# Optimization experiments

Hardware: AMD Instinct MI355X
Metric: run time of the kernel (lower is better)

Reference implementation:

```python
import jax, jax.numpy as jnp
import numpy as np

B, S, D = 4, 1024, 1024
E, F, TOPK = 16, 512, 4


def setup_inputs() -> dict:
    key = jax.random.key(0)
    k1, k2, k3, k4, k5 = jax.random.split(key, 5)
    scale = 0.02
    return {
        "x": jax.random.normal(k1, (B, S, D), dtype=jnp.float32),
        "Wr": jax.random.normal(k2, (D, E), dtype=jnp.float32) * scale,   # router
        "Wg": jax.random.normal(k3, (E, D, F), dtype=jnp.float32) * scale,  # gate proj
        "Wu": jax.random.normal(k4, (E, D, F), dtype=jnp.float32) * scale,  # up proj
        "Wd": jax.random.normal(k5, (E, F, D), dtype=jnp.float32) * scale,  # down proj
    }


def reference(x, Wr, Wg, Wu, Wd):
    b, s, d = x.shape
    xf = x.reshape(-1, d)                      # [N, D], N = B*S
    n = xf.shape[0]
    e = Wr.shape[1]

    # --- router: softmax over experts, top-k, renormalized weights ---
    probs = jax.nn.softmax(xf @ Wr, axis=-1)   # [N, E]
    w, idx = jax.lax.top_k(probs, TOPK)        # [N, K], [N, K]
    w = w / jnp.sum(w, axis=-1, keepdims=True)

    # combine weights per (token, expert); zero for unselected experts.
    # Equivalent to the per-expert where/gather/scatter-add loop in torch.
    cw = jnp.zeros((n, e), dtype=xf.dtype).at[jnp.arange(n)[:, None], idx].add(w)

    # --- per-expert gated FFN (SwiGLU), combined with routing weights ---
    def body(acc, ws):
        wg, wu, wd, c = ws                     # [D,F], [D,F], [F,D], [N]
        h = jax.nn.silu(xf @ wg) * (xf @ wu)   # [N, F]
        return acc + c[:, None] * (h @ wd), None

    out, _ = jax.lax.scan(body, jnp.zeros_like(xf), (Wg, Wu, Wd, cw.T))
    return out.reshape(b, s, d)
```

## Files before the change

### kernel.cpp

```cpp
#include <hip/hip_runtime.h>

#define N_TOK 4096
#define DIM   1024
#define NE    16
#define NF    512
#define TOPK  4
#define CAP   4096
#define NPAIR (N_TOK * TOPK)
#define MAXTILES 144

typedef _Float16 v8h __attribute__((ext_vector_type(8)));
typedef float    v4f __attribute__((ext_vector_type(4)));

__global__ __launch_bounds__(64) void router_kernel(
    const float* __restrict__ x, const float* __restrict__ Wr,
    int* __restrict__ tokIdx, float* __restrict__ tokW,
    unsigned short* __restrict__ xb)
{
    int t = blockIdx.x;
    int l = threadIdx.x;
    double z[NE];
#pragma unroll
    for (int e = 0; e < NE; e++) z[e] = 0.0;
    const float* xrow = x + (size_t)t * DIM;
#pragma unroll
    for (int i = 0; i < 16; i++) {
        int d = i * 64 + l;
        double xv = (double)xrow[d];
        const float4* wr = (const float4*)(Wr + d * NE);
        float4 w0 = wr[0], w1 = wr[1], w2 = wr[2], w3 = wr[3];
        z[0]  += xv * w0.x; z[1]  += xv * w0.y; z[2]  += xv * w0.z; z[3]  += xv * w0.w;
        z[4]  += xv * w1.x; z[5]  += xv * w1.y; z[6]  += xv * w1.z; z[7]  += xv * w1.w;
        z[8]  += xv * w2.x; z[9]  += xv * w2.y; z[10] += xv * w2.z; z[11] += xv * w2.w;
        z[12] += xv * w3.x; z[13] += xv * w3.y; z[14] += xv * w3.z; z[15] += xv * w3.w;
    }
    const float4* xv4 = (const float4*)xrow;
#pragma unroll
    for (int h2 = 0; h2 < 2; h2++) {
        int base = h2 * 512 + l * 8;
        float4 a = xv4[h2 * 128 + l * 2];
        float4 b = xv4[h2 * 128 + l * 2 + 1];
        union { unsigned short u[8]; uint4 v; } p;
        p.u[0] = __builtin_bit_cast(unsigned short, (_Float16)a.x);
        p.u[1] = __builtin_bit_cast(unsigned short, (_Float16)a.y);
        p.u[2] = __builtin_bit_cast(unsigned short, (_Float16)a.z);
        p.u[3] = __builtin_bit_cast(unsigned short, (_Float16)a.w);
        p.u[4] = __builtin_bit_cast(unsigned short, (_Float16)b.x);
        p.u[5] = __builtin_bit_cast(unsigned short, (_Float16)b.y);
        p.u[6] = __builtin_bit_cast(unsigned short, (_Float16)b.z);
        p.u[7] = __builtin_bit_cast(unsigned short, (_Float16)b.w);
        *(uint4*)(xb + (size_t)t * DIM + base) = p.v;
    }
#pragma unroll
    for (int e = 0; e < NE; e++) {
#pragma unroll
        for (int m = 1; m < 64; m <<= 1) z[e] += __shfl_xor(z[e], m, 64);
    }
    if (l == 0) {
        bool taken[NE];
#pragma unroll
        for (int e = 0; e < NE; e++) taken[e] = false;
        int idx[TOPK]; double sel[TOPK];
        for (int k = 0; k < TOPK; k++) {
            int bi = 0; double bv = -1.0e300;
            for (int e = 0; e < NE; e++)
                if (!taken[e] && z[e] > bv) { bv = z[e]; bi = e; }
            taken[bi] = true; idx[k] = bi; sel[k] = bv;
        }
        double m = sel[0];
        double ex[TOPK]; double s = 0.0;
        for (int k = 0; k < TOPK; k++) { ex[k] = exp(sel[k] - m); s += ex[k]; }
        for (int k = 0; k < TOPK; k++) {
            tokIdx[t * TOPK + k] = idx[k];
            tokW[t * TOPK + k]   = (float)(ex[k] / s);
        }
    }
}

__global__ __launch_bounds__(256) void bin_kernel(
    const int* __restrict__ tokIdx,
    int* __restrict__ cnt, int* __restrict__ bpair)
{
    int e = blockIdx.x;
    int tid = threadIdx.x, lane = tid & 63, wv = tid >> 6;
    __shared__ int wsum[4];
    __shared__ int sbase;
    if (tid == 0) sbase = 0;
    __syncthreads();
    unsigned long long lt = (1ULL << lane) - 1ULL;
#pragma unroll 1
    for (int c0 = 0; c0 < NPAIR; c0 += 1024) {
        int i0 = c0 + tid * 4;
        int4 v = *(const int4*)(tokIdx + i0);
        int m[4] = {v.x == e, v.y == e, v.z == e, v.w == e};
        int r[4]; int wcnt = 0;
#pragma unroll
        for (int j = 0; j < 4; j++) {
            unsigned long long bal = __ballot(m[j] != 0);
            r[j] = wcnt + __popcll(bal & lt);
            wcnt += __popcll(bal);
        }
        if (lane == 0) wsum[wv] = wcnt;
        __syncthreads();
        int woff = sbase;
        for (int k = 0; k < wv; k++) woff += wsum[k];
#pragma unroll
        for (int j = 0; j < 4; j++)
            if (m[j]) bpair[e * CAP + woff + r[j]] = i0 + j;
        __syncthreads();
        if (tid == 0) sbase += wsum[0] + wsum[1] + wsum[2] + wsum[3];
        __syncthreads();
    }
    if (tid == 0) cnt[e] = sbase;
}

__global__ __launch_bounds__(256) void prep_weight_kernel(
    const float* __restrict__ Wg, const float* __restrict__ Wu,
    const float* __restrict__ Wd,
    unsigned short* __restrict__ Wg_t, unsigned short* __restrict__ Wu_t,
    unsigned short* __restrict__ Wd_t)
{
    int z = blockIdx.y;
    int which = z >> 4, e = z & 15;
    const float* src; unsigned short* dst; int R, C, RIL;
    if (which == 0)      { src = Wg; dst = Wg_t; R = DIM; C = NF;  RIL = 6; }
    else if (which == 1) { src = Wu; dst = Wu_t; R = DIM; C = NF;  RIL = 6; }
    else                 { src = Wd; dst = Wd_t; R = NF;  C = DIM; RIL = 7; }
    int bx = blockIdx.x;
    int cbl, rbl;
    if (which < 2) { cbl = bx & 7;  rbl = bx >> 3; }
    else           { cbl = bx & 15; rbl = bx >> 4; }
    int c0 = cbl * 64, r0 = rbl * 64;

    __shared__ float tile[64][65];
    const float* s = src + (size_t)e * R * C;
    int t = threadIdx.x;
    int tr = t >> 4, tc = (t & 15) * 4;
#pragma unroll
    for (int i = 0; i < 4; i++) {
        int row = i * 16 + tr;
        float4 v = *(const float4*)(s + (size_t)(r0 + row) * C + c0 + tc);
        tile[row][tc + 0] = v.x; tile[row][tc + 1] = v.y;
        tile[row][tc + 2] = v.z; tile[row][tc + 3] = v.w;
    }
    __syncthreads();
    int ktPerE = R >> 5;
    int cbPerE = C >> RIL;
    int imgSz  = (1 << RIL) * 32;
#pragma unroll
    for (int i = 0; i < 4; i++) {
        int nr = i * 16 + tr;
        int orow = c0 + nr;
        int k0 = r0 + tc;
        int cb = orow >> RIL;
        int r  = orow & ((1 << RIL) - 1);
        int kt = k0 >> 5;
        size_t off = ((size_t)(e * cbPerE + cb) * ktPerE + kt) * imgSz
                   + r * 32 + (k0 & 31);
        union { unsigned short u[4]; uint2 v; } p;
#pragma unroll
        for (int j = 0; j < 4; j++)
            p.u[j] = __builtin_bit_cast(unsigned short, (_Float16)tile[tc + j][nr]);
        *(uint2*)(dst + off) = p.v;
    }
}

__device__ __forceinline__ int ldsw(int row, int chunk) {
    return row * 32 + (chunk ^ ((row >> 1) & 3)) * 8;
}

__device__ __forceinline__ bool find_tile(const int* __restrict__ cnt,
                                          int ti, int& e, int& mt, int& tbase) {
    int rt = 0;
#pragma unroll 1
    for (int ee = 0; ee < NE; ee++) {
        int nt = (cnt[ee] + 127) >> 7;
        if (ti < rt + nt) { e = ee; mt = ti - rt; tbase = rt; return true; }
        rt += nt;
    }
    return false;
}

__global__ __launch_bounds__(256) void ffn_gate_up_kernel(
    const unsigned short* __restrict__ xb,
    const unsigned short* __restrict__ Wg_t,
    const unsigned short* __restrict__ Wu_t,
    const int* __restrict__ cnt,
    const int* __restrict__ bpair,
    unsigned short* __restrict__ h_t)
{
    int fb = blockIdx.x, ti = blockIdx.y;
    int e, mt, tbase;
    if (!find_tile(cnt, ti, e, mt, tbase)) return;
    int count = cnt[e];

    __shared__ __align__(16) unsigned short sX[128 * 32];
    __shared__ __align__(16) unsigned short sG[64 * 32];
    __shared__ __align__(16) unsigned short sU[64 * 32];
    __shared__ int sTok[128];

    int tid = threadIdx.x, lane = tid & 63, w = tid >> 6;
    if (tid < 128) {
        int pos = mt * 128 + tid;
        sTok[tid] = bpair[e * CAP + min(pos, count - 1)] >> 2;
    }
    __syncthreads();

    int xr0 = tid >> 2, xc = tid & 3;
    int xr1 = xr0 + 64;
    const unsigned short* gx0 = xb + (size_t)sTok[xr0] * DIM + xc * 8;
    const unsigned short* gx1 = xb + (size_t)sTok[xr1] * DIM + xc * 8;
    const unsigned short* gsrc = Wg_t + ((size_t)(e * 8 + fb) * 32) * 2048 + tid * 8;
    const unsigned short* usrc = Wu_t + ((size_t)(e * 8 + fb) * 32) * 2048 + tid * 8;

    unsigned short* wx0 = &sX[ldsw(xr0, xc)];
    unsigned short* wx1 = &sX[ldsw(xr1, xc)];
    unsigned short* wg  = &sG[ldsw(xr0, xc)];
    unsigned short* wu  = &sU[ldsw(xr0, xc)];

    int row = lane & 15, q = lane >> 4;
    int rw = w & 1, cw = w >> 1;
    int aoff[4], goff[2];
#pragma unroll
    for (int mi = 0; mi < 4; mi++) aoff[mi] = ldsw(rw * 64 + mi * 16 + row, q);
#pragma unroll
    for (int ni = 0; ni < 2; ni++) goff[ni] = ldsw(cw * 32 + ni * 16 + row, q);

    v4f accG[4][2], accU[4][2];
    v4f zero = {0.f, 0.f, 0.f, 0.f};
#pragma unroll
    for (int mi = 0; mi < 4; mi++)
#pragma unroll
        for (int ni = 0; ni < 2; ni++) { accG[mi][ni] = zero; accU[mi][ni] = zero; }

    uint4 rx0 = *(const uint4*)(gx0);
    uint4 rx1 = *(const uint4*)(gx1);
    uint4 rg  = *(const uint4*)(gsrc);
    uint4 ru  = *(const uint4*)(usrc);

#pragma unroll 1
    for (int kt = 0; kt < 32; kt++) {
        __syncthreads();
        *(uint4*)wx0 = rx0;
        *(uint4*)wx1 = rx1;
        *(uint4*)wg  = rg;
        *(uint4*)wu  = ru;
        if (kt < 31) {
            rx0 = *(const uint4*)(gx0 + (kt + 1) * 32);
            rx1 = *(const uint4*)(gx1 + (kt + 1) * 32);
            rg  = *(const uint4*)(gsrc + (size_t)(kt + 1) * 2048);
            ru  = *(const uint4*)(usrc + (size_t)(kt + 1) * 2048);
        }
        __syncthreads();
        v8h a[4], bg[2], bu[2];
#pragma unroll
        for (int mi = 0; mi < 4; mi++) a[mi] = *(const v8h*)&sX[aoff[mi]];
#pragma unroll
        for (int ni = 0; ni < 2; ni++) {
            bg[ni] = *(const v8h*)&sG[goff[ni]];
            bu[ni] = *(const v8h*)&sU[goff[ni]];
        }
#pragma unroll
        for (int mi = 0; mi < 4; mi++)
#pragma unroll
            for (int ni = 0; ni < 2; ni++) {
                accG[mi][ni] = __builtin_amdgcn_mfma_f32_16x16x32_f16(a[mi], bg[ni], accG[mi][ni], 0, 0, 0);
                accU[mi][ni] = __builtin_amdgcn_mfma_f32_16x16x32_f16(a[mi], bu[ni], accU[mi][ni], 0, 0, 0);
            }
    }

    size_t himg = (size_t)(tbase + mt) * 16;
#pragma unroll
    for (int mi = 0; mi < 4; mi++)
#pragma unroll
        for (int ni = 0; ni < 2; ni++) {
            int f = fb * 64 + cw * 32 + ni * 16 + row;
#pragma unroll
            for (int i = 0; i < 4; i++) {
                int rl = rw * 64 + mi * 16 + q * 4 + i;
                int pos = mt * 128 + rl;
                if (pos < count) {
                    float gv = accG[mi][ni][i];
                    float uv = accU[mi][ni][i];
                    float hv = gv * uv / (1.0f + __expf(-gv));
                    size_t off = (himg + (f >> 5)) * 4096 + rl * 32 + (f & 31);
                    h_t[off] = __builtin_bit_cast(unsigned short, (_Float16)hv);
                }
            }
        }
}

__global__ __launch_bounds__(256) void ffn_down_kernel(
    const unsigned short* __restrict__ h_t,
    const unsigned short* __restrict__ Wd_t,
    const int* __restrict__ cnt,
    const int* __restrict__ bpair,
    unsigned short* __restrict__ part)
{
    int ti = blockIdx.x, db = blockIdx.y;
    int e, mt, tbase;
    if (!find_tile(cnt, ti, e, mt, tbase)) return;
    int count = cnt[e];

    __shared__ __align__(16) unsigned short sH[128 * 32];
    __shared__ __align__(16) unsigned short sW[128 * 32];
    __shared__ int sPair[128];

    int tid = threadIdx.x, lane = tid & 63, w = tid >> 6;
    if (tid < 128) {
        int pos = mt * 128 + tid;
        sPair[tid] = bpair[e * CAP + min(pos, count - 1)];
    }
    __syncthreads();

    int r0 = tid >> 2, c = tid & 3;
    int r1 = r0 + 64;
    const unsigned short* hsrc = h_t + ((size_t)(tbase + mt) * 16) * 4096 + tid * 8;
    const unsigned short* wsrc = Wd_t + ((size_t)(e * 8 + db) * 16) * 4096 + tid * 8;

    unsigned short* wh0 = &sH[ldsw(r0, c)];
    unsigned short* wh1 = &sH[ldsw(r1, c)];
    unsigned short* ww0 = &sW[ldsw(r0, c)];
    unsigned short* ww1 = &sW[ldsw(r1, c)];

    int row = lane & 15, q = lane >> 4;
    int rw = w & 1, cw = w >> 1;
    int aoff[4], boff[4];
#pragma unroll
    for (int mi = 0; mi < 4; mi++) aoff[mi] = ldsw(rw * 64 + mi * 16 + row, q);
#pragma unroll
    for (int ni = 0; ni < 4; ni++) boff[ni] = ldsw(cw * 64 + ni * 16 + row, q);

    v4f acc[4][4];
    v4f zero = {0.f, 0.f, 0.f, 0.f};
#pragma unroll
    for (int mi = 0; mi < 4; mi++)
#pragma unroll
        for (int ni = 0; ni < 4; ni++) acc[mi][ni] = zero;

    uint4 rh0 = *(const uint4*)(hsrc);
    uint4 rh1 = *(const uint4*)(hsrc + 2048);
    uint4 rw0 = *(const uint4*)(wsrc);
    uint4 rw1 = *(const uint4*)(wsrc + 2048);

#pragma unroll 1
    for (int kt = 0; kt < 16; kt++) {
        __syncthreads();
        *(uint4*)wh0 = rh0;
        *(uint4*)wh1 = rh1;
        *(uint4*)ww0 = rw0;
        *(uint4*)ww1 = rw1;
        if (kt < 15) {
            rh0 = *(const uint4*)(hsrc + (size_t)(kt + 1) * 4096);
            rh1 = *(const uint4*)(hsrc + (size_t)(kt + 1) * 4096 + 2048);
            rw0 = *(const uint4*)(wsrc + (size_t)(kt + 1) * 4096);
            rw1 = *(const uint4*)(wsrc + (size_t)(kt + 1) * 4096 + 2048);
        }
        __syncthreads();
        v8h a[4], b[4];
#pragma unroll
        for (int mi = 0; mi < 4; mi++) a[mi] = *(const v8h*)&sH[aoff[mi]];
#pragma unroll
        for (int ni = 0; ni < 4; ni++) b[ni] = *(const v8h*)&sW[boff[ni]];
#pragma unroll
        for (int mi = 0; mi < 4; mi++)
#pragma unroll
            for (int ni = 0; ni < 4; ni++)
                acc[mi][ni] = __builtin_amdgcn_mfma_f32_16x16x32_f16(a[mi], b[ni], acc[mi][ni], 0, 0, 0);
    }

#pragma unroll
    for (int mi = 0; mi < 4; mi++)
#pragma unroll
        for (int ni = 0; ni < 4; ni++) {
            int col = db * 128 + cw * 64 + ni * 16 + row;
#pragma unroll
            for (int i = 0; i < 4; i++) {
                int rl = rw * 64 + mi * 16 + q * 4 + i;
                int pos = mt * 128 + rl;
                if (pos < count) {
                    int p = sPair[rl];
                    part[(size_t)p * DIM + col] =
                        __builtin_bit_cast(unsigned short, (_Float16)acc[mi][ni][i]);
                }
            }
        }
}

__global__ __launch_bounds__(256) void combine_kernel(
    const unsigned short* __restrict__ part, const float* __restrict__ tokW,
    float* __restrict__ out)
{
    int gid = blockIdx.x * 256 + threadIdx.x;
    int t = gid >> 8;
    int c = (gid & 255) * 4;
    float4 r = {0.f, 0.f, 0.f, 0.f};
#pragma unroll
    for (int k = 0; k < TOPK; k++) {
        float wk = tokW[t * TOPK + k];
        union { uint2 u; _Float16 h[4]; } cv;
        cv.u = *(const uint2*)(part + ((size_t)(t * TOPK + k)) * DIM + c);
        r.x += wk * (float)cv.h[0];
        r.y += wk * (float)cv.h[1];
        r.z += wk * (float)cv.h[2];
        r.w += wk * (float)cv.h[3];
    }
    *(float4*)(out + (size_t)t * DIM + c) = r;
}

extern "C" void kernel_launch(void* const* d_in, const int* in_sizes, int n_in,
                              void* d_out, int out_size, void* d_ws, size_t ws_size,
                              hipStream_t stream)
{
    const float* x  = (const float*)d_in[0];
    const float* Wr = (const float*)d_in[1];
    const float* Wg = (const float*)d_in[2];
    const float* Wu = (const float*)d_in[3];
    const float* Wd = (const float*)d_in[4];
    float* out = (float*)d_out;
    char* ws = (char*)d_ws;

    size_t off = 0;
    int* tokIdx = (int*)(ws + off);   off += (size_t)NPAIR * 4;
    float* tokW = (float*)(ws + off); off += (size_t)NPAIR * 4;
    int* cnt    = (int*)(ws + off);   off += 256;
    int* bpair  = (int*)(ws + off);   off += (size_t)NE * CAP * 4;
    unsigned short* xb   = (unsigned short*)(ws + off); off += (size_t)N_TOK * DIM * 2;
    unsigned short* Wg_t = (unsigned short*)(ws + off); off += (size_t)NE * DIM * NF * 2;
    unsigned short* Wu_t = (unsigned short*)(ws + off); off += (size_t)NE * DIM * NF * 2;
    unsigned short* Wd_t = (unsigned short*)(ws + off); off += (size_t)NE * DIM * NF * 2;
    unsigned short* h_t  = (unsigned short*)(ws + off); off += (size_t)MAXTILES * 16 * 4096 * 2;
    unsigned short* part = (unsigned short*)(ws + off); off += (size_t)NPAIR * DIM * 2;

    router_kernel<<<N_TOK, 64, 0, stream>>>(x, Wr, tokIdx, tokW, xb);
    bin_kernel<<<NE, 256, 0, stream>>>(tokIdx, cnt, bpair);
    prep_weight_kernel<<<dim3(128, 48), 256, 0, stream>>>(Wg, Wu, Wd, Wg_t, Wu_t, Wd_t);
    ffn_gate_up_kernel<<<dim3(8, MAXTILES), 256, 0, stream>>>(
        xb, Wg_t, Wu_t, cnt, bpair, h_t);
    ffn_down_kernel<<<dim3(MAXTILES, 8), 256, 0, stream>>>(
        h_t, Wd_t, cnt, bpair, part);
    combine_kernel<<<(N_TOK * DIM) / (256 * 4), 256, 0, stream>>>(part, tokW, out);
}
```

Baseline: 286.9 us.

## Use direct global-to-LDS loads with double-buffered shared tiles in FFN kernels

```diff
diff --git a/kernel.cpp b/kernel.cpp
--- a/kernel.cpp
+++ b/kernel.cpp
@@ -169,6 +169,12 @@
     return row * 32 + (chunk ^ ((row >> 1) & 3)) * 8;
 }
 
+__device__ __forceinline__ void gload16(const unsigned short* g, unsigned short* l) {
+    __builtin_amdgcn_global_load_lds(
+        (const __attribute__((address_space(1))) void*)g,
+        (__attribute__((address_space(3))) void*)l, 16, 0, 0);
+}
+
 __device__ __forceinline__ bool find_tile(const int* __restrict__ cnt,
                                           int ti, int& e, int& mt, int& tbase) {
     int rt = 0;
@@ -194,9 +200,9 @@
     if (!find_tile(cnt, ti, e, mt, tbase)) return;
     int count = cnt[e];
 
-    __shared__ __align__(16) unsigned short sX[128 * 32];
-    __shared__ __align__(16) unsigned short sG[64 * 32];
-    __shared__ __align__(16) unsigned short sU[64 * 32];
+    __shared__ __align__(16) unsigned short sX[2 * 128 * 32];
+    __shared__ __align__(16) unsigned short sG[2 * 64 * 32];
+    __shared__ __align__(16) unsigned short sU[2 * 64 * 32];
     __shared__ int sTok[128];
 
     int tid = threadIdx.x, lane = tid & 63, w = tid >> 6;
@@ -206,17 +212,19 @@
     }
     __syncthreads();
 
-    int xr0 = tid >> 2, xc = tid & 3;
-    int xr1 = xr0 + 64;
-    const unsigned short* gx0 = xb + (size_t)sTok[xr0] * DIM + xc * 8;
-    const unsigned short* gx1 = xb + (size_t)sTok[xr1] * DIM + xc * 8;
-    const unsigned short* gsrc = Wg_t + ((size_t)(e * 8 + fb) * 32) * 2048 + tid * 8;
-    const unsigned short* usrc = Wu_t + ((size_t)(e * 8 + fb) * 32) * 2048 + tid * 8;
-
-    unsigned short* wx0 = &sX[ldsw(xr0, xc)];
-    unsigned short* wx1 = &sX[ldsw(xr1, xc)];
-    unsigned short* wg  = &sG[ldsw(xr0, xc)];
-    unsigned short* wu  = &sU[ldsw(xr0, xc)];
+    int srow0 = w * 16 + (lane >> 2);
+    int srow1 = srow0 + 64;
+    int spos  = lane & 3;
+    int cx0 = spos ^ ((srow0 >> 1) & 3);
+    int cx1 = spos ^ ((srow1 >> 1) & 3);
+    const unsigned short* gX0 = xb + (size_t)sTok[srow0] * DIM + cx0 * 8;
+    const unsigned short* gX1 = xb + (size_t)sTok[srow1] * DIM + cx1 * 8;
+    const unsigned short* gG  = Wg_t + ((size_t)(e * 8 + fb) * 32) * 2048 + srow0 * 32 + cx0 * 8;
+    const unsigned short* gU  = Wu_t + ((size_t)(e * 8 + fb) * 32) * 2048 + srow0 * 32 + cx0 * 8;
+    unsigned short* dX0 = sX + (size_t)(w * 16) * 32;
+    unsigned short* dX1 = sX + (size_t)(64 + w * 16) * 32;
+    unsigned short* dG  = sG + (size_t)(w * 16) * 32;
+    unsigned short* dU  = sU + (size_t)(w * 16) * 32;
 
     int row = lane & 15, q = lane >> 4;
     int rw = w & 1, cw = w >> 1;
@@ -233,32 +241,30 @@
 #pragma unroll
         for (int ni = 0; ni < 2; ni++) { accG[mi][ni] = zero; accU[mi][ni] = zero; }
 
-    uint4 rx0 = *(const uint4*)(gx0);
-    uint4 rx1 = *(const uint4*)(gx1);
-    uint4 rg  = *(const uint4*)(gsrc);
-    uint4 ru  = *(const uint4*)(usrc);
+#define STAGE_GU(b, kt) do {                                   \
+        gload16(gX0 + (kt) * 32, dX0 + (b) * 4096);            \
+        gload16(gX1 + (kt) * 32, dX1 + (b) * 4096);            \
+        gload16(gG + (size_t)(kt) * 2048, dG + (b) * 2048);    \
+        gload16(gU + (size_t)(kt) * 2048, dU + (b) * 2048);    \
+    } while (0)
+
+    STAGE_GU(0, 0);
+    __syncthreads();
 
 #pragma unroll 1
     for (int kt = 0; kt < 32; kt++) {
-        __syncthreads();
-        *(uint4*)wx0 = rx0;
-        *(uint4*)wx1 = rx1;
-        *(uint4*)wg  = rg;
-        *(uint4*)wu  = ru;
-        if (kt < 31) {
-            rx0 = *(const uint4*)(gx0 + (kt + 1) * 32);
-            rx1 = *(const uint4*)(gx1 + (kt + 1) * 32);
-            rg  = *(const uint4*)(gsrc + (size_t)(kt + 1) * 2048);
-            ru  = *(const uint4*)(usrc + (size_t)(kt + 1) * 2048);
-        }
-        __syncthreads();
+        int buf = kt & 1;
+        if (kt < 31) STAGE_GU(buf ^ 1, kt + 1);
+        const unsigned short* bX = sX + buf * 4096;
+        const unsigned short* bGp = sG + buf * 2048;
+        const unsigned short* bUp = sU + buf * 2048;
         v8h a[4], bg[2], bu[2];
 #pragma unroll
-        for (int mi = 0; mi < 4; mi++) a[mi] = *(const v8h*)&sX[aoff[mi]];
+        for (int mi = 0; mi < 4; mi++) a[mi] = *(const v8h*)&bX[aoff[mi]];
 #pragma unroll
         for (int ni = 0; ni < 2; ni++) {
-            bg[ni] = *(const v8h*)&sG[goff[ni]];
-            bu[ni] = *(const v8h*)&sU[goff[ni]];
+            bg[ni] = *(const v8h*)&bGp[goff[ni]];
+            bu[ni] = *(const v8h*)&bUp[goff[ni]];
         }
 #pragma unroll
         for (int mi = 0; mi < 4; mi++)
@@ -267,7 +273,9 @@
                 accG[mi][ni] = __builtin_amdgcn_mfma_f32_16x16x32_f16(a[mi], bg[ni], accG[mi][ni], 0, 0, 0);
                 accU[mi][ni] = __builtin_amdgcn_mfma_f32_16x16x32_f16(a[mi], bu[ni], accU[mi][ni], 0, 0, 0);
             }
-    }
+        __syncthreads();
+    }
+#undef STAGE_GU
 
     size_t himg = (size_t)(tbase + mt) * 16;
 #pragma unroll
@@ -302,8 +310,8 @@
     if (!find_tile(cnt, ti, e, mt, tbase)) return;
     int count = cnt[e];
 
-    __shared__ __align__(16) unsigned short sH[128 * 32];
-    __shared__ __align__(16) unsigned short sW[128 * 32];
+    __shared__ __align__(16) unsigned short sH[2 * 128 * 32];
+    __shared__ __align__(16) unsigned short sW[2 * 128 * 32];
     __shared__ int sPair[128];
 
     int tid = threadIdx.x, lane = tid & 63, w = tid >> 6;
@@ -313,15 +321,21 @@
     }
     __syncthreads();
 
-    int r0 = tid >> 2, c = tid & 3;
-    int r1 = r0 + 64;
-    const unsigned short* hsrc = h_t + ((size_t)(tbase + mt) * 16) * 4096 + tid * 8;
-    const unsigned short* wsrc = Wd_t + ((size_t)(e * 8 + db) * 16) * 4096 + tid * 8;
-
-    unsigned short* wh0 = &sH[ldsw(r0, c)];
-    unsigned short* wh1 = &sH[ldsw(r1, c)];
-    unsigned short* ww0 = &sW[ldsw(r0, c)];
-    unsigned short* ww1 = &sW[ldsw(r1, c)];
+    int srow0 = w * 16 + (lane >> 2);
+    int srow1 = srow0 + 64;
+    int spos  = lane & 3;
+    int c0 = spos ^ ((srow0 >> 1) & 3);
+    int c1 = spos ^ ((srow1 >> 1) & 3);
+    const unsigned short* hbase = h_t + ((size_t)(tbase + mt) * 16) * 4096;
+    const unsigned short* wbase = Wd_t + ((size_t)(e * 8 + db) * 16) * 4096;
+    const unsigned short* gH0 = hbase + srow0 * 32 + c0 * 8;
+    const unsigned short* gH1 = hbase + srow1 * 32 + c1 * 8;
+    const unsigned short* gW0 = wbase + srow0 * 32 + c0 * 8;
+    const unsigned short* gW1 = wbase + srow1 * 32 + c1 * 8;
+    unsigned short* dH0 = sH + (size_t)(w * 16) * 32;
+    unsigned short* dH1 = sH + (size_t)(64 + w * 16) * 32;
+    unsigned short* dW0 = sW + (size_t)(w * 16) * 32;
+    unsigned short* dW1 = sW + (size_t)(64 + w * 16) * 32;
 
     int row = lane & 15, q = lane >> 4;
     int rw = w & 1, cw = w >> 1;
@@ -338,36 +352,35 @@
 #pragma unroll
         for (int ni = 0; ni < 4; ni++) acc[mi][ni] = zero;
 
-    uint4 rh0 = *(const uint4*)(hsrc);
-    uint4 rh1 = *(const uint4*)(hsrc + 2048);
-    uint4 rw0 = *(const uint4*)(wsrc);
-    uint4 rw1 = *(const uint4*)(wsrc + 2048);
+#define STAGE_D(b, kt) do {                                         \
+        gload16(gH0 + (size_t)(kt) * 4096, dH0 + (b) * 4096);       \
+        gload16(gH1 + (size_t)(kt) * 4096, dH1 + (b) * 4096);       \
+        gload16(gW0 + (size_t)(kt) * 4096, dW0 + (b) * 4096);       \
+        gload16(gW1 + (size_t)(kt) * 4096, dW1 + (b) * 4096);       \
+    } while (0)
+
+    STAGE_D(0, 0);
+    __syncthreads();
 
 #pragma unroll 1
     for (int kt = 0; kt < 16; kt++) {
-        __syncthreads();
-        *(uint4*)wh0 = rh0;
-        *(uint4*)wh1 = rh1;
-        *(uint4*)ww0 = rw0;
-        *(uint4*)ww1 = rw1;
-        if (kt < 15) {
-            rh0 = *(const uint4*)(hsrc + (size_t)(kt + 1) * 4096);
-            rh1 = *(const uint4*)(hsrc + (size_t)(kt + 1) * 4096 + 2048);
-            rw0 = *(const uint4*)(wsrc + (size_t)(kt + 1) * 4096);
-            rw1 = *(const uint4*)(wsrc + (size_t)(kt + 1) * 4096 + 2048);
-        }
-        __syncthreads();
+        int buf = kt & 1;
+        if (kt < 15) STAGE_D(buf ^ 1, kt + 1);
+        const unsigned short* bH = sH + buf * 4096;
+        const unsigned short* bW = sW + buf * 4096;
         v8h a[4], b[4];
 #pragma unroll
-        for (int mi = 0; mi < 4; mi++) a[mi] = *(const v8h*)&sH[aoff[mi]];
-#pragma unroll
-        for (int ni = 0; ni < 4; ni++) b[ni] = *(const v8h*)&sW[boff[ni]];
+        for (int mi = 0; mi < 4; mi++) a[mi] = *(const v8h*)&bH[aoff[mi]];
+#pragma unroll
+        for (int ni = 0; ni < 4; ni++) b[ni] = *(const v8h*)&bW[boff[ni]];
 #pragma unroll
         for (int mi = 0; mi < 4; mi++)
 #pragma unroll
             for (int ni = 0; ni < 4; ni++)
                 acc[mi][ni] = __builtin_amdgcn_mfma_f32_16x16x32_f16(a[mi], b[ni], acc[mi][ni], 0, 0, 0);
-    }
+        __syncthreads();
+    }
+#undef STAGE_D
 
 #pragma unroll
     for (int mi = 0; mi < 4; mi++)
```

New measurement: 294.5 us. 1.03x slower.
